# Performance work log

Measured on AMD Instinct MI355X. Metric: run time of the kernel, lower is better.

Reference implementation:

```python
import jax, jax.numpy as jnp
import numpy as np

EPS = 1e-5
BLEND = 0.5  # with prior_batchsize=0, x_iclm == x_bn so CNM == BatchNorm1d (training mode)


def batchnorm(x, gamma, beta):
    # torch BatchNorm1d training mode: batch mean, biased variance
    mean = x.mean(axis=0)
    var = x.var(axis=0)  # ddof=0 (biased), matching torch normalization
    xn = (x - mean) * jax.lax.rsqrt(var + EPS)
    return xn * gamma + beta


def ensemble_linear(x, W):
    # x: [B, D*F], W: [D, O, F] block-diagonal weights
    B = x.shape[0]
    D, O, F = W.shape
    xb = x.reshape(B, D, F)
    out = jnp.einsum('bdf,dof->bdo', xb, W)
    return out.reshape(B, D * O)


def setup_inputs() -> dict:
    key = jax.random.key(0)
    ks = jax.random.split(key, 3)
    B, F, D, O2 = 16384, 1024, 4, 32
    x = jax.random.normal(ks[0], (B, F), dtype=jnp.float32)
    # torch init: normal_(mean=0, std=0.0001) on linear weights
    W1 = jax.random.normal(ks[1], (D, F, F), dtype=jnp.float32) * 1e-4
    W2 = jax.random.normal(ks[2], (D, O2, F), dtype=jnp.float32) * 1e-4
    g1 = jnp.ones((D * F,), jnp.float32); b1 = jnp.zeros((D * F,), jnp.float32)
    g2 = jnp.ones((D * F,), jnp.float32); b2 = jnp.zeros((D * F,), jnp.float32)
    g3 = jnp.ones((D * O2,), jnp.float32); b3 = jnp.zeros((D * O2,), jnp.float32)
    return {"x": x, "W1": W1, "W2": W2, "g1": g1, "b1": b1,
            "g2": g2, "b2": b2, "g3": g3, "b3": b3}


def reference(x, W1, W2, g1, b1, g2, b2, g3, b3):
    D = W1.shape[0]
    h = jnp.concatenate([x] * D, axis=-1)          # [B, D*F]
    h = batchnorm(h, g1, b1)                        # CNM 1
    h = ensemble_linear(h, W1)                      # EnsembleLinear F->F
    h = jax.nn.sigmoid(batchnorm(h, g2, b2))        # CNM 2 + Sigmoid
    h = ensemble_linear(h, W2)                      # EnsembleLinear F->32
    h = jax.nn.sigmoid(batchnorm(h, g3, b3))        # CNM 3 + Sigmoid
    return h  # [B, D*32]
```

## Files before the change

### kernel.cpp

```cpp
#include <hip/hip_runtime.h>
#include <hip/hip_bf16.h>
#include <stdint.h>

#define B_N 16384
#define F_N 1024
#define D_N 4
#define O_N 32
#define NCOL1 (D_N * F_N)
#define NCOL2 (D_N * O_N)

static constexpr float EPS = 1e-5f;

typedef __bf16 bf16x8 __attribute__((ext_vector_type(8)));
typedef __bf16 bf16x4 __attribute__((ext_vector_type(4)));
typedef float  f32x4  __attribute__((ext_vector_type(4)));

#define GLD16(gp, lp)                                                          \
  __builtin_amdgcn_global_load_lds(                                            \
      (__attribute__((address_space(1))) void*)(uintptr_t)(gp),                \
      (__attribute__((address_space(3))) void*)(lp), 16, 0, 0)

__global__ __launch_bounds__(256) void k_stats_x_partial(
    const float* __restrict__ x, float* __restrict__ part) {
  int t = threadIdx.x, blk = blockIdx.x;
  const float4* xr = (const float4*)x;
  float s0 = 0, s1 = 0, s2 = 0, s3 = 0, q0 = 0, q1 = 0, q2 = 0, q3 = 0;
  int r0 = blk * 128;
  for (int r = r0; r < r0 + 128; ++r) {
    float4 v = xr[(size_t)r * (F_N / 4) + t];
    s0 += v.x; q0 += v.x * v.x;
    s1 += v.y; q1 += v.y * v.y;
    s2 += v.z; q2 += v.z * v.z;
    s3 += v.w; q3 += v.w * v.w;
  }
  float* p = part + (size_t)blk * 2048;
  p[t * 4 + 0] = s0; p[t * 4 + 1] = s1; p[t * 4 + 2] = s2; p[t * 4 + 3] = s3;
  p[1024 + t * 4 + 0] = q0; p[1024 + t * 4 + 1] = q1;
  p[1024 + t * 4 + 2] = q2; p[1024 + t * 4 + 3] = q3;
}

__global__ __launch_bounds__(256) void k_stats_x_final(
    const float* __restrict__ part, float* __restrict__ meanx,
    float* __restrict__ rstdx) {
  int c = blockIdx.x * 256 + threadIdx.x;
  float s = 0, q = 0;
  for (int b = 0; b < 128; ++b) {
    s += part[(size_t)b * 2048 + c];
    q += part[(size_t)b * 2048 + 1024 + c];
  }
  float mean = s * (1.0f / B_N);
  float var = q * (1.0f / B_N) - mean * mean;
  meanx[c] = mean;
  rstdx[c] = rsqrtf(var + EPS);
}

__global__ __launch_bounds__(256) void k_fold_w1(const float* __restrict__ W1,
                                                 const float* __restrict__ g1,
                                                 __bf16* __restrict__ W1b) {
  size_t base = (size_t)(blockIdx.x * 256 + threadIdx.x) * 4;
  int f = (int)(base & (F_N - 1));
  int d = (int)(base >> 20);
  float4 w = *(const float4*)(W1 + base);
  float4 g = *(const float4*)(g1 + d * F_N + f);
  bf16x4 o;
  o[0] = (__bf16)(w.x * g.x); o[1] = (__bf16)(w.y * g.y);
  o[2] = (__bf16)(w.z * g.z); o[3] = (__bf16)(w.w * g.w);
  *(bf16x4*)(W1b + base) = o;
}

__global__ __launch_bounds__(256) void k_fold_w2(const float* __restrict__ W2,
                                                 __bf16* __restrict__ W2b) {
  size_t base = (size_t)(blockIdx.x * 256 + threadIdx.x) * 4;
  float4 w = *(const float4*)(W2 + base);
  bf16x4 o;
  o[0] = (__bf16)w.x; o[1] = (__bf16)w.y; o[2] = (__bf16)w.z; o[3] = (__bf16)w.w;
  *(bf16x4*)(W2b + base) = o;
}

__global__ __launch_bounds__(256) void k_make_xn(const float* __restrict__ x,
                                                 const float* __restrict__ meanx,
                                                 const float* __restrict__ rstdx,
                                                 __bf16* __restrict__ xn) {
  size_t base = (size_t)(blockIdx.x * 256 + threadIdx.x) * 4;
  int f = (int)(base & (F_N - 1));
  float4 v = *(const float4*)(x + base);
  float4 m = *(const float4*)(meanx + f);
  float4 r = *(const float4*)(rstdx + f);
  bf16x4 o;
  o[0] = (__bf16)((v.x - m.x) * r.x);
  o[1] = (__bf16)((v.y - m.y) * r.y);
  o[2] = (__bf16)((v.z - m.z) * r.z);
  o[3] = (__bf16)((v.w - m.w) * r.w);
  *(bf16x4*)(xn + base) = o;
}

__global__ __launch_bounds__(256) void k_gemm1(const __bf16* __restrict__ A,
                                               const __bf16* __restrict__ Bw,
                                               __bf16* __restrict__ C) {
  __shared__ __bf16 Asm[128 * 32];
  __shared__ __bf16 Bsm[128 * 32];
  const int tid = threadIdx.x;
  const int wave = tid >> 6, lane = tid & 63;
  const int m0 = blockIdx.x * 128, n0 = blockIdx.y * 128;
  const int srow = tid >> 2;
  const int scol = (tid & 3) * 8;
  const __bf16* Ag = A + (size_t)(m0 + srow) * F_N + scol;
  const __bf16* Bg = Bw + (size_t)(n0 + srow) * F_N + scol;
  __bf16* AsBase = &Asm[wave * 512];
  __bf16* BsBase = &Bsm[wave * 512];
  const int fr = lane & 15, fk = (lane >> 4) * 8;
  const int awr = (wave >> 1) * 64, awc = (wave & 1) * 64;
  f32x4 acc[4][4] = {};
  for (int k0 = 0; k0 < F_N; k0 += 32) {
    __syncthreads();
    GLD16(Ag + k0, AsBase);
    GLD16(Ag + (size_t)64 * F_N + k0, AsBase + 2048);
    GLD16(Bg + k0, BsBase);
    GLD16(Bg + (size_t)64 * F_N + k0, BsBase + 2048);
    __syncthreads();
    bf16x8 af[4], bfr[4];
#pragma unroll
    for (int mi = 0; mi < 4; ++mi)
      af[mi] = *(const bf16x8*)&Asm[(awr + mi * 16 + fr) * 32 + fk];
#pragma unroll
    for (int ni = 0; ni < 4; ++ni)
      bfr[ni] = *(const bf16x8*)&Bsm[(awc + ni * 16 + fr) * 32 + fk];
#pragma unroll
    for (int mi = 0; mi < 4; ++mi)
#pragma unroll
      for (int ni = 0; ni < 4; ++ni)
        acc[mi][ni] = __builtin_amdgcn_mfma_f32_16x16x32_bf16(
            af[mi], bfr[ni], acc[mi][ni], 0, 0, 0);
  }
  const int cr = (lane >> 4) * 4, cc = lane & 15;
#pragma unroll
  for (int mi = 0; mi < 4; ++mi)
#pragma unroll
    for (int ni = 0; ni < 4; ++ni) {
      int row = m0 + awr + mi * 16 + cr;
      int col = n0 + awc + ni * 16 + cc;
#pragma unroll
      for (int r = 0; r < 4; ++r)
        C[(size_t)(row + r) * NCOL1 + col] = (__bf16)acc[mi][ni][r];
    }
}

__global__ __launch_bounds__(256) void k_stats2_partial(
    const __bf16* __restrict__ G1, float* __restrict__ part) {
  int t = threadIdx.x, blk = blockIdx.x;
  float s[16], q[16];
#pragma unroll
  for (int j = 0; j < 16; ++j) { s[j] = 0; q[j] = 0; }
  int r0 = blk * 128;
  for (int r = r0; r < r0 + 128; ++r) {
    const __bf16* row = G1 + (size_t)r * NCOL1 + t * 16;
    bf16x8 v0 = *(const bf16x8*)row;
    bf16x8 v1 = *(const bf16x8*)(row + 8);
#pragma unroll
    for (int j = 0; j < 8; ++j) { float f = (float)v0[j]; s[j] += f; q[j] += f * f; }
#pragma unroll
    for (int j = 0; j < 8; ++j) { float f = (float)v1[j]; s[8 + j] += f; q[8 + j] += f * f; }
  }
  float* p = part + (size_t)blk * 8192;
#pragma unroll
  for (int j = 0; j < 16; ++j) {
    p[t * 16 + j] = s[j];
    p[4096 + t * 16 + j] = q[j];
  }
}

__global__ __launch_bounds__(256) void k_stats2_final(
    const float* __restrict__ part, const float* __restrict__ g2,
    const float* __restrict__ b2, float* __restrict__ a2,
    float* __restrict__ c2) {
  int c = blockIdx.x * 256 + threadIdx.x;
  float s = 0, q = 0;
  for (int b = 0; b < 128; ++b) {
    s += part[(size_t)b * 8192 + c];
    q += part[(size_t)b * 8192 + 4096 + c];
  }
  float mean = s * (1.0f / B_N);
  float var = q * (1.0f / B_N) - mean * mean;
  float rstd = rsqrtf(var + EPS);
  float aa = rstd * g2[c];
  a2[c] = aa;
  c2[c] = b2[c] - mean * aa;
}

__global__ __launch_bounds__(256) void k_gemm2(
    const __bf16* __restrict__ G1, const __bf16* __restrict__ W2b,
    const float* __restrict__ a2, const float* __restrict__ c2,
    float* __restrict__ out2) {
  const int tid = threadIdx.x;
  const int wave = tid >> 6, lane = tid & 63;
  const int m0 = blockIdx.x * 64;
  const int d = blockIdx.y;
  const int fr = lane & 15, fk = (lane >> 4) * 8;
  const __bf16* Arow = G1 + (size_t)(m0 + wave * 16 + fr) * NCOL1 + d * F_N;
  const __bf16* Wd = W2b + (size_t)d * O_N * F_N;
  const float* ap = a2 + d * F_N;
  const float* cp = c2 + d * F_N;
  f32x4 acc[2] = {};
  for (int k0 = 0; k0 < F_N; k0 += 32) {
    bf16x8 av = *(const bf16x8*)(Arow + k0 + fk);
    f32x4 aa0 = *(const f32x4*)(ap + k0 + fk);
    f32x4 aa1 = *(const f32x4*)(ap + k0 + fk + 4);
    f32x4 cc0 = *(const f32x4*)(cp + k0 + fk);
    f32x4 cc1 = *(const f32x4*)(cp + k0 + fk + 4);
    bf16x8 af;
#pragma unroll
    for (int j = 0; j < 4; ++j) {
      float v = (float)av[j] * aa0[j] + cc0[j];
      af[j] = (__bf16)(1.0f / (1.0f + __expf(-v)));
    }
#pragma unroll
    for (int j = 0; j < 4; ++j) {
      float v = (float)av[4 + j] * aa1[j] + cc1[j];
      af[4 + j] = (__bf16)(1.0f / (1.0f + __expf(-v)));
    }
    bf16x8 b0 = *(const bf16x8*)(Wd + (size_t)fr * F_N + k0 + fk);
    bf16x8 b1 = *(const bf16x8*)(Wd + (size_t)(16 + fr) * F_N + k0 + fk);
    acc[0] = __builtin_amdgcn_mfma_f32_16x16x32_bf16(af, b0, acc[0], 0, 0, 0);
    acc[1] = __builtin_amdgcn_mfma_f32_16x16x32_bf16(af, b1, acc[1], 0, 0, 0);
  }
  const int cr = (lane >> 4) * 4, cc = lane & 15;
#pragma unroll
  for (int n = 0; n < 2; ++n)
#pragma unroll
    for (int r = 0; r < 4; ++r)
      out2[(size_t)(m0 + wave * 16 + cr + r) * NCOL2 + d * O_N + n * 16 + cc] =
          acc[n][r];
}

__global__ __launch_bounds__(128) void k_stats3_partial(
    const float* __restrict__ out2, float* __restrict__ part) {
  int t = threadIdx.x, blk = blockIdx.x;
  float s = 0, q = 0;
  int r0 = blk * 128;
  for (int r = r0; r < r0 + 128; ++r) {
    float v = out2[(size_t)r * NCOL2 + t];
    s += v;
    q += v * v;
  }
  part[(size_t)blk * 256 + t] = s;
  part[(size_t)blk * 256 + 128 + t] = q;
}

__global__ __launch_bounds__(128) void k_stats3_final(
    const float* __restrict__ part, const float* __restrict__ g3,
    const float* __restrict__ b3, float* __restrict__ a3,
    float* __restrict__ c3) {
  int c = threadIdx.x;
  float s = 0, q = 0;
  for (int b = 0; b < 128; ++b) {
    s += part[(size_t)b * 256 + c];
    q += part[(size_t)b * 256 + 128 + c];
  }
  float mean = s * (1.0f / B_N);
  float var = q * (1.0f / B_N) - mean * mean;
  float rstd = rsqrtf(var + EPS);
  float aa = rstd * g3[c];
  a3[c] = aa;
  c3[c] = b3[c] - mean * aa;
}

__global__ __launch_bounds__(256) void k_final(const float* __restrict__ out2,
                                               const float* __restrict__ a3,
                                               const float* __restrict__ c3,
                                               float* __restrict__ out) {
  size_t base = (size_t)(blockIdx.x * 256 + threadIdx.x) * 4;
  int c = (int)(base & (NCOL2 - 1));
  f32x4 v = *(const f32x4*)(out2 + base);
  f32x4 a = *(const f32x4*)(a3 + c);
  f32x4 cc = *(const f32x4*)(c3 + c);
  f32x4 o;
#pragma unroll
  for (int j = 0; j < 4; ++j)
    o[j] = 1.0f / (1.0f + __expf(-(v[j] * a[j] + cc[j])));
  *(f32x4*)(out + base) = o;
}

extern "C" void kernel_launch(void* const* d_in, const int* in_sizes, int n_in,
                              void* d_out, int out_size, void* d_ws,
                              size_t ws_size, hipStream_t stream) {
  (void)in_sizes; (void)n_in; (void)out_size; (void)ws_size;
  const float* x = (const float*)d_in[0];
  const float* W1 = (const float*)d_in[1];
  const float* W2 = (const float*)d_in[2];
  const float* g1 = (const float*)d_in[3];
  const float* g2 = (const float*)d_in[5];
  const float* b2 = (const float*)d_in[6];
  const float* g3 = (const float*)d_in[7];
  const float* b3 = (const float*)d_in[8];
  float* out = (float*)d_out;

  char* ws = (char*)d_ws;
  size_t off = 0;
  auto alloc = [&](size_t bytes) -> void* {
    void* p = ws + off;
    off = (off + bytes + 255) & ~(size_t)255;
    return p;
  };
  float* meanx = (float*)alloc((size_t)F_N * 4);
  float* rstdx = (float*)alloc((size_t)F_N * 4);
  float* a2 = (float*)alloc((size_t)NCOL1 * 4);
  float* c2 = (float*)alloc((size_t)NCOL1 * 4);
  float* a3 = (float*)alloc((size_t)NCOL2 * 4);
  float* c3 = (float*)alloc((size_t)NCOL2 * 4);
  float* part1 = (float*)alloc((size_t)128 * 2048 * 4);
  float* part2 = (float*)alloc((size_t)128 * 8192 * 4);
  float* part3 = (float*)alloc((size_t)128 * 256 * 4);
  __bf16* W1b = (__bf16*)alloc((size_t)D_N * F_N * F_N * 2);
  __bf16* W2b = (__bf16*)alloc((size_t)D_N * O_N * F_N * 2);
  __bf16* xn = (__bf16*)alloc((size_t)B_N * F_N * 2);
  __bf16* G1 = (__bf16*)alloc((size_t)B_N * NCOL1 * 2);
  float* out2 = (float*)alloc((size_t)B_N * NCOL2 * 4);

  k_stats_x_partial<<<128, 256, 0, stream>>>(x, part1);
  k_stats_x_final<<<4, 256, 0, stream>>>(part1, meanx, rstdx);
  k_fold_w1<<<4096, 256, 0, stream>>>(W1, g1, W1b);
  k_fold_w2<<<128, 256, 0, stream>>>(W2, W2b);
  k_make_xn<<<16384, 256, 0, stream>>>(x, meanx, rstdx, xn);
  k_gemm1<<<dim3(128, 32), 256, 0, stream>>>(xn, W1b, G1);
  k_stats2_partial<<<128, 256, 0, stream>>>(G1, part2);
  k_stats2_final<<<16, 256, 0, stream>>>(part2, g2, b2, a2, c2);
  k_gemm2<<<dim3(256, 4), 256, 0, stream>>>(G1, W2b, a2, c2, out2);
  k_stats3_partial<<<128, 128, 0, stream>>>(out2, part3);
  k_stats3_final<<<1, 128, 0, stream>>>(part3, g3, b3, a3, c3);
  k_final<<<2048, 256, 0, stream>>>(out2, a3, c3, out);
}
```

Measured before the change: 329.2 us.

## Fold BN1 into W1, fuse stats2 into a pipelined 256x256 gemm1

Removes the separate normalized-x pass. x is cast to bf16 inside the stats kernel and rstd is folded into W1; the mean is dropped because the later batchnorm cancels any per-column shift. GEMM1 becomes a 512-thread, 256x256-tile, double-buffered kernel with block swizzling, priority hints and manual waitcnt scheduling. Its epilogue emits per-column sum and sum-of-squares partials, so the separate G1 stats read is gone. Skipping the mean subtraction changes bf16 rounding and the variance could lose precision if inputs have large means.

```diff
diff --git a/kernel.cpp b/kernel.cpp
--- a/kernel.cpp
+++ b/kernel.cpp
@@ -20,8 +20,9 @@
       (__attribute__((address_space(1))) void*)(uintptr_t)(gp),                \
       (__attribute__((address_space(3))) void*)(lp), 16, 0, 0)
 
-__global__ __launch_bounds__(256) void k_stats_x_partial(
-    const float* __restrict__ x, float* __restrict__ part) {
+__global__ __launch_bounds__(256) void k_stats_x_conv(
+    const float* __restrict__ x, float* __restrict__ part,
+    __bf16* __restrict__ xb) {
   int t = threadIdx.x, blk = blockIdx.x;
   const float4* xr = (const float4*)x;
   float s0 = 0, s1 = 0, s2 = 0, s3 = 0, q0 = 0, q1 = 0, q2 = 0, q3 = 0;
@@ -32,6 +33,9 @@
     s1 += v.y; q1 += v.y * v.y;
     s2 += v.z; q2 += v.z * v.z;
     s3 += v.w; q3 += v.w * v.w;
+    bf16x4 o;
+    o[0] = (__bf16)v.x; o[1] = (__bf16)v.y; o[2] = (__bf16)v.z; o[3] = (__bf16)v.w;
+    *(bf16x4*)(xb + (size_t)r * F_N + t * 4) = o;
   }
   float* p = part + (size_t)blk * 2048;
   p[t * 4 + 0] = s0; p[t * 4 + 1] = s1; p[t * 4 + 2] = s2; p[t * 4 + 3] = s3;
@@ -40,8 +44,7 @@
 }
 
 __global__ __launch_bounds__(256) void k_stats_x_final(
-    const float* __restrict__ part, float* __restrict__ meanx,
-    float* __restrict__ rstdx) {
+    const float* __restrict__ part, float* __restrict__ rstdx) {
   int c = blockIdx.x * 256 + threadIdx.x;
   float s = 0, q = 0;
   for (int b = 0; b < 128; ++b) {
@@ -50,21 +53,22 @@
   }
   float mean = s * (1.0f / B_N);
   float var = q * (1.0f / B_N) - mean * mean;
-  meanx[c] = mean;
   rstdx[c] = rsqrtf(var + EPS);
 }
 
 __global__ __launch_bounds__(256) void k_fold_w1(const float* __restrict__ W1,
                                                  const float* __restrict__ g1,
+                                                 const float* __restrict__ rstdx,
                                                  __bf16* __restrict__ W1b) {
   size_t base = (size_t)(blockIdx.x * 256 + threadIdx.x) * 4;
   int f = (int)(base & (F_N - 1));
   int d = (int)(base >> 20);
   float4 w = *(const float4*)(W1 + base);
   float4 g = *(const float4*)(g1 + d * F_N + f);
+  float4 r = *(const float4*)(rstdx + f);
   bf16x4 o;
-  o[0] = (__bf16)(w.x * g.x); o[1] = (__bf16)(w.y * g.y);
-  o[2] = (__bf16)(w.z * g.z); o[3] = (__bf16)(w.w * g.w);
+  o[0] = (__bf16)(w.x * g.x * r.x); o[1] = (__bf16)(w.y * g.y * r.y);
+  o[2] = (__bf16)(w.z * g.z * r.z); o[3] = (__bf16)(w.w * g.w * r.w);
   *(bf16x4*)(W1b + base) = o;
 }
 
@@ -77,107 +81,144 @@
   *(bf16x4*)(W2b + base) = o;
 }
 
-__global__ __launch_bounds__(256) void k_make_xn(const float* __restrict__ x,
-                                                 const float* __restrict__ meanx,
-                                                 const float* __restrict__ rstdx,
-                                                 __bf16* __restrict__ xn) {
-  size_t base = (size_t)(blockIdx.x * 256 + threadIdx.x) * 4;
-  int f = (int)(base & (F_N - 1));
-  float4 v = *(const float4*)(x + base);
-  float4 m = *(const float4*)(meanx + f);
-  float4 r = *(const float4*)(rstdx + f);
-  bf16x4 o;
-  o[0] = (__bf16)((v.x - m.x) * r.x);
-  o[1] = (__bf16)((v.y - m.y) * r.y);
-  o[2] = (__bf16)((v.z - m.z) * r.z);
-  o[3] = (__bf16)((v.w - m.w) * r.w);
-  *(bf16x4*)(xn + base) = o;
-}
-
-__global__ __launch_bounds__(256) void k_gemm1(const __bf16* __restrict__ A,
-                                               const __bf16* __restrict__ Bw,
-                                               __bf16* __restrict__ C) {
-  __shared__ __bf16 Asm[128 * 32];
-  __shared__ __bf16 Bsm[128 * 32];
+__global__ __launch_bounds__(512, 2) void k_gemm1(
+    const __bf16* __restrict__ A, const __bf16* __restrict__ Bw,
+    __bf16* __restrict__ C, float* __restrict__ p2s, float* __restrict__ p2q) {
+  __shared__ __bf16 ldsA[2][2][256 * 32];
+  __shared__ __bf16 ldsB[2][2][256 * 32];
   const int tid = threadIdx.x;
   const int wave = tid >> 6, lane = tid & 63;
-  const int m0 = blockIdx.x * 128, n0 = blockIdx.y * 128;
+  const int wm = wave >> 2, wn = wave & 3;
+  int bid = (int)blockIdx.x;
+  int swz = (bid & 7) * 128 + (bid >> 3);
+  const int bm = swz & 63, bn = swz >> 6;
+  const int m0 = bm * 256, n0 = bn * 256;
+  const int fr = lane & 15, kg = lane >> 4;
   const int srow = tid >> 2;
-  const int scol = (tid & 3) * 8;
-  const __bf16* Ag = A + (size_t)(m0 + srow) * F_N + scol;
-  const __bf16* Bg = Bw + (size_t)(n0 + srow) * F_N + scol;
-  __bf16* AsBase = &Asm[wave * 512];
-  __bf16* BsBase = &Bsm[wave * 512];
-  const int fr = lane & 15, fk = (lane >> 4) * 8;
-  const int awr = (wave >> 1) * 64, awc = (wave & 1) * 64;
-  f32x4 acc[4][4] = {};
-  for (int k0 = 0; k0 < F_N; k0 += 32) {
-    __syncthreads();
-    GLD16(Ag + k0, AsBase);
-    GLD16(Ag + (size_t)64 * F_N + k0, AsBase + 2048);
-    GLD16(Bg + k0, BsBase);
-    GLD16(Bg + (size_t)64 * F_N + k0, BsBase + 2048);
-    __syncthreads();
-    bf16x8 af[4], bfr[4];
-#pragma unroll
-    for (int mi = 0; mi < 4; ++mi)
-      af[mi] = *(const bf16x8*)&Asm[(awr + mi * 16 + fr) * 32 + fk];
-#pragma unroll
-    for (int ni = 0; ni < 4; ++ni)
-      bfr[ni] = *(const bf16x8*)&Bsm[(awc + ni * 16 + fr) * 32 + fk];
-#pragma unroll
-    for (int mi = 0; mi < 4; ++mi)
-#pragma unroll
-      for (int ni = 0; ni < 4; ++ni)
-        acc[mi][ni] = __builtin_amdgcn_mfma_f32_16x16x32_bf16(
-            af[mi], bfr[ni], acc[mi][ni], 0, 0, 0);
-  }
-  const int cr = (lane >> 4) * 4, cc = lane & 15;
-#pragma unroll
-  for (int mi = 0; mi < 4; ++mi)
+  const int scb = (tid & 3) * 16;
+  const char* Ab = (const char*)A + (size_t)(m0 + srow) * (F_N * 2) + scb;
+  const char* Bb = (const char*)Bw + (size_t)(n0 + srow) * (F_N * 2) + scb;
+  char* ldsAx = (char*)&ldsA[0][0][0];
+  char* ldsBx = (char*)&ldsB[0][0][0];
+  const int wo = wave * 1024;
+
+#define SA(buf_, kk_, kb_)                                                     \
+  do {                                                                         \
+    GLD16(Ab + (kb_) + (kk_) * 64,                                             \
+          ldsAx + (buf_) * 32768 + (kk_) * 16384 + wo);                        \
+    GLD16(Ab + 128 * (F_N * 2) + (kb_) + (kk_) * 64,                           \
+          ldsAx + (buf_) * 32768 + (kk_) * 16384 + 8192 + wo);                 \
+  } while (0)
+#define SBv(buf_, kk_, kb_)                                                    \
+  do {                                                                         \
+    GLD16(Bb + (kb_) + (kk_) * 64,                                             \
+          ldsBx + (buf_) * 32768 + (kk_) * 16384 + wo);                        \
+    GLD16(Bb + 128 * (F_N * 2) + (kb_) + (kk_) * 64,                           \
+          ldsBx + (buf_) * 32768 + (kk_) * 16384 + 8192 + wo);                 \
+  } while (0)
+#define LDA4(buf_, kk_, qm_)                                                   \
+  { _Pragma("unroll") for (int i_ = 0; i_ < 4; ++i_)                           \
+      afr[i_] = *(const bf16x8*)&ldsA[buf_][kk_]                               \
+          [(wm * 128 + (qm_) * 64 + i_ * 16 + fr) * 32 + kg * 8]; }
+#define LDB4(buf_, kk_)                                                        \
+  { _Pragma("unroll") for (int i_ = 0; i_ < 4; ++i_)                           \
+      bfr[i_] = *(const bf16x8*)&ldsB[buf_][kk_]                               \
+          [(wn * 64 + i_ * 16 + fr) * 32 + kg * 8]; }
+#define MFMA16(qm_)                                                            \
+  { _Pragma("unroll") for (int i_ = 0; i_ < 4; ++i_)                           \
+      _Pragma("unroll") for (int j_ = 0; j_ < 4; ++j_)                         \
+        acc[(qm_) * 4 + i_][j_] = __builtin_amdgcn_mfma_f32_16x16x32_bf16(     \
+            afr[i_], bfr[j_], acc[(qm_) * 4 + i_][j_], 0, 0, 0); }
+#define BAR() __builtin_amdgcn_s_barrier()
+#define WAITLGKM()                                                             \
+  do {                                                                         \
+    asm volatile("s_waitcnt lgkmcnt(0)" ::: "memory");                         \
+    __builtin_amdgcn_sched_barrier(0);                                         \
+  } while (0)
+#define WAITVM4() asm volatile("s_waitcnt vmcnt(4)" ::: "memory")
+#define PRIO1() __builtin_amdgcn_s_setprio(1)
+#define PRIO0() __builtin_amdgcn_s_setprio(0)
+
+  f32x4 acc[8][4] = {};
+  bf16x8 afr[4], bfr[4];
+
+  SBv(0, 0, 0); SA(0, 0, 0); SBv(0, 1, 0); SA(0, 1, 0);
+  asm volatile("s_waitcnt vmcnt(4)" ::: "memory");
+  BAR();
+
+  for (int t = 0; t < 16; t += 2) {
+    const int kn1 = (t + 1) * 128;
+    const int kn2 = (t + 2 < 16) ? (t + 2) * 128 : 0;
+    LDA4(0, 0, 0); LDB4(0, 0); SBv(1, 0, kn1); BAR(); WAITLGKM(); PRIO1(); MFMA16(0); PRIO0(); BAR();
+    LDA4(0, 0, 1);             SA (1, 0, kn1); BAR(); WAITLGKM(); PRIO1(); MFMA16(1); PRIO0(); WAITVM4(); BAR();
+    LDA4(0, 1, 0); LDB4(0, 1); SBv(1, 1, kn1); BAR(); WAITLGKM(); PRIO1(); MFMA16(0); PRIO0(); BAR();
+    LDA4(0, 1, 1);             SA (1, 1, kn1); BAR(); WAITLGKM(); PRIO1(); MFMA16(1); PRIO0(); WAITVM4(); BAR();
+    LDA4(1, 0, 0); LDB4(1, 0); SBv(0, 0, kn2); BAR(); WAITLGKM(); PRIO1(); MFMA16(0); PRIO0(); BAR();
+    LDA4(1, 0, 1);             SA (0, 0, kn2); BAR(); WAITLGKM(); PRIO1(); MFMA16(1); PRIO0(); WAITVM4(); BAR();
+    LDA4(1, 1, 0); LDB4(1, 1); SBv(0, 1, kn2); BAR(); WAITLGKM(); PRIO1(); MFMA16(0); PRIO0(); BAR();
+    LDA4(1, 1, 1);             SA (0, 1, kn2); BAR(); WAITLGKM(); PRIO1(); MFMA16(1); PRIO0(); WAITVM4(); BAR();
+  }
+
+  const int cr = kg * 4, cc = fr;
+#pragma unroll
+  for (int mi = 0; mi < 8; ++mi)
 #pragma unroll
     for (int ni = 0; ni < 4; ++ni) {
-      int row = m0 + awr + mi * 16 + cr;
-      int col = n0 + awc + ni * 16 + cc;
+      int row = m0 + wm * 128 + mi * 16 + cr;
+      int col = n0 + wn * 64 + ni * 16 + cc;
 #pragma unroll
       for (int r = 0; r < 4; ++r)
         C[(size_t)(row + r) * NCOL1 + col] = (__bf16)acc[mi][ni][r];
     }
-}
-
-__global__ __launch_bounds__(256) void k_stats2_partial(
-    const __bf16* __restrict__ G1, float* __restrict__ part) {
-  int t = threadIdx.x, blk = blockIdx.x;
-  float s[16], q[16];
-#pragma unroll
-  for (int j = 0; j < 16; ++j) { s[j] = 0; q[j] = 0; }
-  int r0 = blk * 128;
-  for (int r = r0; r < r0 + 128; ++r) {
-    const __bf16* row = G1 + (size_t)r * NCOL1 + t * 16;
-    bf16x8 v0 = *(const bf16x8*)row;
-    bf16x8 v1 = *(const bf16x8*)(row + 8);
-#pragma unroll
-    for (int j = 0; j < 8; ++j) { float f = (float)v0[j]; s[j] += f; q[j] += f * f; }
-#pragma unroll
-    for (int j = 0; j < 8; ++j) { float f = (float)v1[j]; s[8 + j] += f; q[8 + j] += f * f; }
-  }
-  float* p = part + (size_t)blk * 8192;
-#pragma unroll
-  for (int j = 0; j < 16; ++j) {
-    p[t * 16 + j] = s[j];
-    p[4096 + t * 16 + j] = q[j];
-  }
+
+  float* srs = (float*)&ldsA[1][0][0];
+  float* srq = srs + 512;
+  __syncthreads();
+#pragma unroll
+  for (int ni = 0; ni < 4; ++ni) {
+    float ss = 0, qq = 0;
+#pragma unroll
+    for (int mi = 0; mi < 8; ++mi) {
+      f32x4 v = acc[mi][ni];
+#pragma unroll
+      for (int r = 0; r < 4; ++r) { ss += v[r]; qq += v[r] * v[r]; }
+    }
+    ss += __shfl_xor(ss, 16); ss += __shfl_xor(ss, 32);
+    qq += __shfl_xor(qq, 16); qq += __shfl_xor(qq, 32);
+    if (lane < 16) {
+      srs[wave * 64 + ni * 16 + lane] = ss;
+      srq[wave * 64 + ni * 16 + lane] = qq;
+    }
+  }
+  __syncthreads();
+  if (tid < 256) {
+    int j = tid, wnn = j >> 6, jj = j & 63;
+    float S = srs[wnn * 64 + jj] + srs[(4 + wnn) * 64 + jj];
+    float Q = srq[wnn * 64 + jj] + srq[(4 + wnn) * 64 + jj];
+    p2s[(size_t)bm * NCOL1 + n0 + j] = S;
+    p2q[(size_t)bm * NCOL1 + n0 + j] = Q;
+  }
+#undef SA
+#undef SBv
+#undef LDA4
+#undef LDB4
+#undef MFMA16
+#undef BAR
+#undef WAITLGKM
+#undef WAITVM4
+#undef PRIO1
+#undef PRIO0
 }
 
 __global__ __launch_bounds__(256) void k_stats2_final(
-    const float* __restrict__ part, const float* __restrict__ g2,
-    const float* __restrict__ b2, float* __restrict__ a2,
-    float* __restrict__ c2) {
+    const float* __restrict__ p2s, const float* __restrict__ p2q,
+    const float* __restrict__ g2, const float* __restrict__ b2,
+    float* __restrict__ a2, float* __restrict__ c2) {
   int c = blockIdx.x * 256 + threadIdx.x;
   float s = 0, q = 0;
-  for (int b = 0; b < 128; ++b) {
-    s += part[(size_t)b * 8192 + c];
-    q += part[(size_t)b * 8192 + 4096 + c];
+  for (int b = 0; b < 64; ++b) {
+    s += p2s[(size_t)b * NCOL1 + c];
+    q += p2q[(size_t)b * NCOL1 + c];
   }
   float mean = s * (1.0f / B_N);
   float var = q * (1.0f / B_N) - mean * mean;
@@ -301,29 +342,27 @@
     off = (off + bytes + 255) & ~(size_t)255;
     return p;
   };
-  float* meanx = (float*)alloc((size_t)F_N * 4);
   float* rstdx = (float*)alloc((size_t)F_N * 4);
   float* a2 = (float*)alloc((size_t)NCOL1 * 4);
   float* c2 = (float*)alloc((size_t)NCOL1 * 4);
   float* a3 = (float*)alloc((size_t)NCOL2 * 4);
   float* c3 = (float*)alloc((size_t)NCOL2 * 4);
   float* part1 = (float*)alloc((size_t)128 * 2048 * 4);
-  float* part2 = (float*)alloc((size_t)128 * 8192 * 4);
+  float* p2s = (float*)alloc((size_t)64 * NCOL1 * 4);
+  float* p2q = (float*)alloc((size_t)64 * NCOL1 * 4);
   float* part3 = (float*)alloc((size_t)128 * 256 * 4);
   __bf16* W1b = (__bf16*)alloc((size_t)D_N * F_N * F_N * 2);
   __bf16* W2b = (__bf16*)alloc((size_t)D_N * O_N * F_N * 2);
-  __bf16* xn = (__bf16*)alloc((size_t)B_N * F_N * 2);
+  __bf16* xb = (__bf16*)alloc((size_t)B_N * F_N * 2);
   __bf16* G1 = (__bf16*)alloc((size_t)B_N * NCOL1 * 2);
   float* out2 = (float*)alloc((size_t)B_N * NCOL2 * 4);
 
-  k_stats_x_partial<<<128, 256, 0, stream>>>(x, part1);
-  k_stats_x_final<<<4, 256, 0, stream>>>(part1, meanx, rstdx);
-  k_fold_w1<<<4096, 256, 0, stream>>>(W1, g1, W1b);
+  k_stats_x_conv<<<128, 256, 0, stream>>>(x, part1, xb);
+  k_stats_x_final<<<4, 256, 0, stream>>>(part1, rstdx);
+  k_fold_w1<<<4096, 256, 0, stream>>>(W1, g1, rstdx, W1b);
   k_fold_w2<<<128, 256, 0, stream>>>(W2, W2b);
-  k_make_xn<<<16384, 256, 0, stream>>>(x, meanx, rstdx, xn);
-  k_gemm1<<<dim3(128, 32), 256, 0, stream>>>(xn, W1b, G1);
-  k_stats2_partial<<<128, 256, 0, stream>>>(G1, part2);
-  k_stats2_final<<<16, 256, 0, stream>>>(part2, g2, b2, a2, c2);
+  k_gemm1<<<1024, 512, 0, stream>>>(xb, W1b, G1, p2s, p2q);
+  k_stats2_final<<<16, 256, 0, stream>>>(p2s, p2q, g2, b2, a2, c2);
   k_gemm2<<<dim3(256, 4), 256, 0, stream>>>(G1, W2b, a2, c2, out2);
   k_stats3_partial<<<128, 128, 0, stream>>>(out2, part3);
   k_stats3_final<<<1, 128, 0, stream>>>(part3, g3, b3, a3, c3);
```

Result: faster. 303.7 us (-7.7%).
